# Optimization experiments

Hardware: AMD Instinct MI355X
Metric: run time of the kernel (lower is better)

The kernel has to match this reference:

```python
import jax, jax.numpy as jnp
import numpy as np

N_NODES, N_EDGES, F_IN = 8192, 32768, 16
N_SUB, N_GRAPH = 512, 32
EDGE_DIM, HID = 5, 128
DIMS = [(16, 32), (32, 64), (64, 64)]  # (M_in, M_out) per NNConv layer


def _segment_mean(x, seg, n):
    s = jax.ops.segment_sum(x, seg, num_segments=n)
    c = jax.ops.segment_sum(jnp.ones((x.shape[0], 1), x.dtype), seg, num_segments=n)
    return s / jnp.maximum(c, 1.0)


def _nnconv(x, src, dst, eattr, W1, b1, W2, b2, root, bias):
    # edge MLP -> per-edge weight matrix theta: [E, M_in, M_out]
    h = jax.nn.relu(eattr @ W1 + b1)
    theta = (h @ W2 + b2).reshape(-1, x.shape[1], root.shape[1])
    msg = jnp.einsum('ei,eio->eo', x[src], theta)          # gather + per-edge matvec
    agg = jax.ops.segment_sum(msg, dst, num_segments=x.shape[0])  # scatter-add (aggr='add')
    return agg + x @ root + bias


def setup_inputs() -> dict:
    key = jax.random.key(0)
    ks = jax.random.split(key, 32)
    inp = {}
    inp['x'] = jax.random.normal(ks[0], (N_NODES, F_IN), jnp.float32)
    inp['edge_index'] = jax.random.randint(ks[1], (2, N_EDGES), 0, N_NODES)
    inp['edge_attr'] = jax.random.uniform(ks[2], (N_EDGES, EDGE_DIM), jnp.float32)
    inp['node_to_subgraph'] = jnp.sort(jax.random.randint(ks[3], (N_NODES,), 0, N_SUB))
    inp['subgraph_to_graph'] = jnp.sort(jax.random.randint(ks[4], (N_SUB,), 0, N_GRAPH))
    i = 5
    for l, (ci, co) in enumerate(DIMS):
        inp[f'W1_{l}'] = jax.random.normal(ks[i], (EDGE_DIM, HID), jnp.float32) * 0.1
        inp[f'b1_{l}'] = jnp.zeros((HID,), jnp.float32)
        inp[f'W2_{l}'] = jax.random.normal(ks[i + 1], (HID, ci * co), jnp.float32) * 0.05
        inp[f'b2_{l}'] = jnp.zeros((ci * co,), jnp.float32)
        inp[f'root_{l}'] = jax.random.normal(ks[i + 2], (ci, co), jnp.float32) * 0.1
        inp[f'bias_{l}'] = jnp.zeros((co,), jnp.float32)
        i += 3
    inp['fc1_w'] = jax.random.normal(ks[i], (64, 32), jnp.float32) * 0.1
    inp['fc1_b'] = jnp.zeros((32,), jnp.float32)
    inp['fc2_w'] = jax.random.normal(ks[i + 1], (32, 16), jnp.float32) * 0.1
    inp['fc2_b'] = jnp.zeros((16,), jnp.float32)
    inp['fc3_w'] = jax.random.normal(ks[i + 2], (16, 1), jnp.float32) * 0.1
    inp['fc3_b'] = jnp.zeros((1,), jnp.float32)
    return inp


def reference(x, edge_index, edge_attr, node_to_subgraph, subgraph_to_graph,
              W1_0, b1_0, W2_0, b2_0, root_0, bias_0,
              W1_1, b1_1, W2_1, b2_1, root_1, bias_1,
              W1_2, b1_2, W2_2, b2_2, root_2, bias_2,
              fc1_w, fc1_b, fc2_w, fc2_b, fc3_w, fc3_b):
    src, dst = edge_index[0], edge_index[1]
    layers = [(W1_0, b1_0, W2_0, b2_0, root_0, bias_0),
              (W1_1, b1_1, W2_1, b2_1, root_1, bias_1),
              (W1_2, b1_2, W2_2, b2_2, root_2, bias_2)]
    h = x
    for (W1, b1, W2, b2, root, bias) in layers:
        h = jax.nn.elu(_nnconv(h, src, dst, edge_attr, W1, b1, W2, b2, root, bias))
    h = _segment_mean(h, node_to_subgraph, N_SUB)      # global_mean_pool over subgraphs
    h = _segment_mean(h, subgraph_to_graph, N_GRAPH)   # global_mean_pool over graphs
    h = jax.nn.elu(h @ fc1_w + fc1_b)
    h = jax.nn.elu(h @ fc2_w + fc2_b)
    return (h @ fc3_w + fc3_b).reshape(-1)
```

## Files before the change

kernel.cpp:

```cpp
#include <hip/hip_runtime.h>

#define E_EDGES 32768
#define NN 8192
#define HID 128
#define KS 4

typedef _Float16 half8 __attribute__((ext_vector_type(8)));
typedef _Float16 half4 __attribute__((ext_vector_type(4)));
typedef float f32x4 __attribute__((ext_vector_type(4)));

__global__ void zero_init_k(int* __restrict__ hist, float* __restrict__ pools, int npool) {
  int t = blockIdx.x * 256 + threadIdx.x;
  if (t < NN) hist[t] = 0;
  if (t < npool) pools[t] = 0.f;
}

__global__ void hist_k(const int* __restrict__ dst, int* __restrict__ hist) {
  int e = blockIdx.x * 256 + threadIdx.x;
  if (e < E_EDGES) atomicAdd(&hist[dst[e]], 1);
}

__global__ void scan_k(const int* __restrict__ hist, int* __restrict__ roff, int* __restrict__ cursor) {
  __shared__ int ps[1024];
  int t = threadIdx.x;
  int loc[8]; int s = 0;
  int base = t * 8;
#pragma unroll
  for (int j = 0; j < 8; ++j) { loc[j] = s; s += hist[base + j]; }
  ps[t] = s;
  __syncthreads();
  for (int off = 1; off < 1024; off <<= 1) {
    int v = 0;
    if (t >= off) v = ps[t - off];
    __syncthreads();
    if (t >= off) ps[t] += v;
    __syncthreads();
  }
  int excl = (t == 0) ? 0 : ps[t - 1];
#pragma unroll
  for (int j = 0; j < 8; ++j) { int v = excl + loc[j]; roff[base + j] = v; cursor[base + j] = v; }
  if (t == 1023) roff[NN] = ps[1023];
}

__global__ void scatter_k(const int* __restrict__ dst, int* __restrict__ cursor, int* __restrict__ eidx) {
  int e = blockIdx.x * 256 + threadIdx.x;
  if (e < E_EDGES) { int p = atomicAdd(&cursor[dst[e]], 1); eidx[p] = e; }
}

template <int CI, int CO>
__global__ void prep_b_k(const float* __restrict__ W2, const float* __restrict__ b2,
                         _Float16* __restrict__ out) {
  constexpr int Kmain = 128 * CI;
  constexpr int SPLITK = 32 * CI;
  constexpr int TAILK = ((SPLITK + CI + 127) / 128) * 128;
  constexpr int Kpad = 3 * SPLITK + TAILK;
  int idx = blockIdx.x * 256 + threadIdx.x;
  if (idx >= Kpad * CO) return;
  int j = idx & 7;
  int n = (idx >> 3) & (CO - 1);
  int kg = idx >> (3 + (CO == 64 ? 6 : 5));
  int k = kg * 8 + j;
  float v = 0.f;
  if (k < Kmain) {
    int h = k / CI, i = k & (CI - 1);
    v = W2[(h * CI + i) * CO + n];
  } else if (k < Kmain + CI) {
    int tt = k - Kmain;
    v = b2[tt * CO + n];
  }
  out[idx] = (_Float16)v;
}

template <int CI, int CO>
__launch_bounds__(256, 2)
__global__ void msg_mfma_k(const float* __restrict__ xcur, const int* __restrict__ src,
                           const float* __restrict__ eattr, const float* __restrict__ W1,
                           const float* __restrict__ b1, const _Float16* __restrict__ Bsw,
                           float* __restrict__ msgbuf) {
  constexpr int ME = 256;
  constexpr int L2CI = (CI == 64) ? 6 : ((CI == 32) ? 5 : 4);
  constexpr int Kmain = 128 * CI;
  constexpr int SPLITK = 32 * CI;
  constexpr int TAILK = ((SPLITK + CI + 127) / 128) * 128;
  constexpr int XSTR = CI + 8;
  constexpr int FC = CO / 16;
  constexpr int C4 = CI / 4;
  constexpr int L2C4 = L2CI - 2;

  __shared__ _Float16 he_s[32 * ME];
  __shared__ _Float16 xs_s[ME * XSTR];
  __shared__ float ea_s[ME * 5];
  __shared__ float W1s[5 * 32];
  __shared__ float b1s[32];
  __shared__ int src_s[ME];

  int t = threadIdx.x;
  int e0 = blockIdx.x * ME;
  int y = blockIdx.y;
  int hbeg = y * 32;

  for (int j = t; j < ME * 5; j += 256) ea_s[j] = eattr[e0 * 5 + j];
  if (t < 5 * 32) W1s[t] = W1[(t >> 5) * HID + hbeg + (t & 31)];
  if (t < 32) b1s[t] = b1[hbeg + t];
  src_s[t] = src[e0 + t];
  __syncthreads();

  for (int j = t; j < 32 * ME; j += 256) {
    int hl = j / ME, e = j & (ME - 1);
    float v = b1s[hl];
#pragma unroll
    for (int d = 0; d < 5; ++d) v += ea_s[e * 5 + d] * W1s[d * 32 + hl];
    he_s[hl * ME + e] = (_Float16)fmaxf(v, 0.f);
  }
  for (int j = t; j < ME * C4; j += 256) {
    int e = j >> L2C4, i4 = j & (C4 - 1);
    float4 v = ((const float4*)xcur)[src_s[e] * C4 + i4];
    half4 hq = {(_Float16)v.x, (_Float16)v.y, (_Float16)v.z, (_Float16)v.w};
    *(half4*)&xs_s[e * XSTR + i4 * 4] = hq;
  }
  __syncthreads();

  int lane = t & 63;
  int w = t >> 6;
  int quad = lane >> 4, l15 = lane & 15;

  int cbeg = y * (SPLITK / 32);
  int cend = cbeg + ((y < 3) ? (SPLITK / 32) : (TAILK / 32));
  int nrounds = (cend - cbeg) >> 2;

  const half8* bsw8 = (const half8*)Bsw;
  int ib = quad * CO + l15;

  f32x4 acc[4][FC];
#pragma unroll
  for (int fr = 0; fr < 4; ++fr)
#pragma unroll
    for (int fc = 0; fc < FC; ++fc)
#pragma unroll
      for (int r = 0; r < 4; ++r) acc[fr][fc][r] = 0.f;

  half8 breg[4][FC];
#pragma unroll
  for (int j = 0; j < 4; ++j)
#pragma unroll
    for (int fc = 0; fc < FC; ++fc)
      breg[j][fc] = bsw8[(cbeg + j) * 4 * CO + ib + fc * 16];

  for (int r = 0; r < nrounds; ++r) {
#pragma unroll
    for (int j = 0; j < 4; ++j) {
      int c = cbeg + r * 4 + j;
      int kq = c * 32 + quad * 8;
      int i = kq & (CI - 1);
      int hr = (kq >> L2CI) - hbeg;
      half8 a[4];
#pragma unroll
      for (int fr = 0; fr < 4; ++fr) {
        int e = w * 64 + fr * 16 + l15;
        half8 xv = *(const half8*)&xs_s[e * XSTR + i];
        _Float16 hv = (_Float16)1.f;
        if (kq < Kmain) hv = he_s[hr * ME + e];
        a[fr] = xv * hv;
      }
#pragma unroll
      for (int fc = 0; fc < FC; ++fc) {
#pragma unroll
        for (int fr = 0; fr < 4; ++fr)
          acc[fr][fc] = __builtin_amdgcn_mfma_f32_16x16x32_f16(a[fr], breg[j][fc], acc[fr][fc], 0, 0, 0);
      }
      int cn = c + 4;
      if (cn >= cend) cn = cend - 1;
#pragma unroll
      for (int fc = 0; fc < FC; ++fc)
        breg[j][fc] = bsw8[cn * 4 * CO + ib + fc * 16];
    }
  }

  float* mb = msgbuf + ((size_t)y * E_EDGES + e0) * CO;
#pragma unroll
  for (int fr = 0; fr < 4; ++fr)
#pragma unroll
    for (int fc = 0; fc < FC; ++fc)
#pragma unroll
      for (int r = 0; r < 4; ++r) {
        int el = w * 64 + fr * 16 + quad * 4 + r;
        int o = fc * 16 + l15;
        mb[el * CO + o] = acc[fr][fc][r];
      }
}

template <int CI, int CO>
__global__ void gather_elu_k(const float* __restrict__ xcur, const float* __restrict__ root,
                             const float* __restrict__ bias, const float* __restrict__ msgbuf,
                             const int* __restrict__ roff, const int* __restrict__ eidx,
                             float* __restrict__ xnext) {
  constexpr int NB = 256 / CO;
  __shared__ float xs[NB * CI];
  int t = threadIdx.x;
  int n0 = blockIdx.x * NB;
  for (int j = t; j < NB * CI; j += 256) xs[j] = xcur[n0 * CI + j];
  __syncthreads();
  int nl = t / CO, o = t & (CO - 1);
  int n = n0 + nl;
  float a = bias[o];
#pragma unroll
  for (int i = 0; i < CI; ++i) a += xs[nl * CI + i] * root[i * CO + o];
  int j1 = roff[n + 1];
  for (int j = roff[n]; j < j1; ++j) {
    int e = eidx[j];
    float m = 0.f;
#pragma unroll
    for (int s = 0; s < KS; ++s) m += msgbuf[((size_t)s * E_EDGES + e) * CO + o];
    a += m;
  }
  xnext[n * CO + o] = a > 0.f ? a : expm1f(a);
}

__global__ void pool_sub_k(const float* __restrict__ x3, const int* __restrict__ n2s,
                           float* __restrict__ ssum, float* __restrict__ scnt) {
  int idx = blockIdx.x * 256 + threadIdx.x;
  int n = idx >> 6, o = idx & 63;
  int s = n2s[n];
  atomicAdd(&ssum[(s << 6) + o], x3[idx]);
  if (o == 0) atomicAdd(&scnt[s], 1.f);
}

__global__ void pool_graph_k(const float* __restrict__ ssum, const float* __restrict__ scnt,
                             const int* __restrict__ s2g, float* __restrict__ gsum,
                             float* __restrict__ gcnt) {
  int idx = blockIdx.x * 256 + threadIdx.x;
  int s = idx >> 6, o = idx & 63;
  int g = s2g[s];
  float v = ssum[idx] / fmaxf(scnt[s], 1.f);
  atomicAdd(&gsum[(g << 6) + o], v);
  if (o == 0) atomicAdd(&gcnt[g], 1.f);
}

__global__ void head_k(const float* __restrict__ gsum, const float* __restrict__ gcnt,
                       const float* __restrict__ w1, const float* __restrict__ b1,
                       const float* __restrict__ w2, const float* __restrict__ b2,
                       const float* __restrict__ w3, const float* __restrict__ b3,
                       float* __restrict__ out) {
  int g = blockIdx.x;
  int t = threadIdx.x;
  __shared__ float m[64], s1[32], s2[16];
  float c = fmaxf(gcnt[g], 1.f);
  m[t] = gsum[g * 64 + t] / c;
  __syncthreads();
  if (t < 32) {
    float a = b1[t];
    for (int i = 0; i < 64; ++i) a += m[i] * w1[i * 32 + t];
    s1[t] = a > 0.f ? a : expm1f(a);
  }
  __syncthreads();
  if (t < 16) {
    float a = b2[t];
    for (int i = 0; i < 32; ++i) a += s1[i] * w2[i * 16 + t];
    s2[t] = a > 0.f ? a : expm1f(a);
  }
  __syncthreads();
  if (t == 0) {
    float a = b3[0];
    for (int i = 0; i < 16; ++i) a += s2[i] * w3[i];
    out[g] = a;
  }
}

extern "C" void kernel_launch(void* const* d_in, const int* in_sizes, int n_in,
                              void* d_out, int out_size, void* d_ws, size_t ws_size,
                              hipStream_t stream) {
  (void)in_sizes; (void)n_in; (void)out_size; (void)ws_size;
  const float* x0 = (const float*)d_in[0];
  const int* ei = (const int*)d_in[1];
  const float* ea = (const float*)d_in[2];
  const int* n2s = (const int*)d_in[3];
  const int* s2g = (const int*)d_in[4];
  const float* W1_[3] = {(const float*)d_in[5], (const float*)d_in[11], (const float*)d_in[17]};
  const float* b1_[3] = {(const float*)d_in[6], (const float*)d_in[12], (const float*)d_in[18]};
  const float* W2_[3] = {(const float*)d_in[7], (const float*)d_in[13], (const float*)d_in[19]};
  const float* b2_[3] = {(const float*)d_in[8], (const float*)d_in[14], (const float*)d_in[20]};
  const float* rt_[3] = {(const float*)d_in[9], (const float*)d_in[15], (const float*)d_in[21]};
  const float* bs_[3] = {(const float*)d_in[10], (const float*)d_in[16], (const float*)d_in[22]};
  const float* fc1w = (const float*)d_in[23]; const float* fc1b = (const float*)d_in[24];
  const float* fc2w = (const float*)d_in[25]; const float* fc2b = (const float*)d_in[26];
  const float* fc3w = (const float*)d_in[27]; const float* fc3b = (const float*)d_in[28];
  float* out = (float*)d_out;

  const int* srcp = ei;
  const int* dstp = ei + E_EDGES;

  char* wsb = (char*)d_ws;
  size_t off = 0;
  auto alloc = [&](size_t bytes) {
    void* p = wsb + off;
    off += (bytes + 255) & ~(size_t)255;
    return p;
  };
  _Float16* Bsw0 = (_Float16*)alloc((size_t)2176 * 32 * 2);
  _Float16* Bsw1 = (_Float16*)alloc((size_t)4224 * 64 * 2);
  _Float16* Bsw2 = (_Float16*)alloc((size_t)8320 * 64 * 2);
  float* msgbuf = (float*)alloc((size_t)KS * E_EDGES * 64 * 4);
  float* x1 = (float*)alloc((size_t)NN * 32 * 4);
  float* x2 = (float*)alloc((size_t)NN * 64 * 4);
  float* x3 = (float*)alloc((size_t)NN * 64 * 4);
  int* hist = (int*)alloc((size_t)NN * 4);
  int* roff = (int*)alloc((size_t)(NN + 1) * 4);
  int* cursor = (int*)alloc((size_t)NN * 4);
  int* eidx = (int*)alloc((size_t)E_EDGES * 4);
  const int npool = 512 * 64 + 512 + 32 * 64 + 32;
  float* pools = (float*)alloc((size_t)npool * 4);
  float* ssum = pools;
  float* scnt = pools + 512 * 64;
  float* gsum = scnt + 512;
  float* gcnt = gsum + 32 * 64;

  zero_init_k<<<(npool + 255) / 256, 256, 0, stream>>>(hist, pools, npool);
  hist_k<<<E_EDGES / 256, 256, 0, stream>>>(dstp, hist);
  scan_k<<<1, 1024, 0, stream>>>(hist, roff, cursor);
  scatter_k<<<E_EDGES / 256, 256, 0, stream>>>(dstp, cursor, eidx);
  prep_b_k<16, 32><<<(2176 * 32 + 255) / 256, 256, 0, stream>>>(W2_[0], b2_[0], Bsw0);
  prep_b_k<32, 64><<<(4224 * 64 + 255) / 256, 256, 0, stream>>>(W2_[1], b2_[1], Bsw1);
  prep_b_k<64, 64><<<(8320 * 64 + 255) / 256, 256, 0, stream>>>(W2_[2], b2_[2], Bsw2);

  dim3 mg(E_EDGES / 256, KS);
  msg_mfma_k<16, 32><<<mg, 256, 0, stream>>>(x0, srcp, ea, W1_[0], b1_[0], Bsw0, msgbuf);
  gather_elu_k<16, 32><<<NN / 8, 256, 0, stream>>>(x0, rt_[0], bs_[0], msgbuf, roff, eidx, x1);
  msg_mfma_k<32, 64><<<mg, 256, 0, stream>>>(x1, srcp, ea, W1_[1], b1_[1], Bsw1, msgbuf);
  gather_elu_k<32, 64><<<NN / 4, 256, 0, stream>>>(x1, rt_[1], bs_[1], msgbuf, roff, eidx, x2);
  msg_mfma_k<64, 64><<<mg, 256, 0, stream>>>(x2, srcp, ea, W1_[2], b1_[2], Bsw2, msgbuf);
  gather_elu_k<64, 64><<<NN / 4, 256, 0, stream>>>(x2, rt_[2], bs_[2], msgbuf, roff, eidx, x3);

  pool_sub_k<<<NN * 64 / 256, 256, 0, stream>>>(x3, n2s, ssum, scnt);
  pool_graph_k<<<512 * 64 / 256, 256, 0, stream>>>(ssum, scnt, s2g, gsum, gcnt);
  head_k<<<32, 64, 0, stream>>>(gsum, gcnt, fc1w, fc1b, fc2w, fc2b, fc3w, fc3b, out);
}
```

Baseline: 269.6 us.

## Fuse CSR build and weight prep kernels, hoist x fragments into registers

Merges zero-init, histogram and scan into one single-block kernel that builds the histogram in shared memory, and merges the three per-layer weight-prep launches into one kernel. This cuts launch count and launch overhead. In the message kernel, each lane's x fragments are loaded from LDS into registers once instead of being reloaded for every K chunk. The cost is a histogram done by one workgroup and extra register pressure.

```diff
diff --git a/kernel.cpp b/kernel.cpp
--- a/kernel.cpp
+++ b/kernel.cpp
@@ -9,24 +9,20 @@
 typedef _Float16 half4 __attribute__((ext_vector_type(4)));
 typedef float f32x4 __attribute__((ext_vector_type(4)));
 
-__global__ void zero_init_k(int* __restrict__ hist, float* __restrict__ pools, int npool) {
-  int t = blockIdx.x * 256 + threadIdx.x;
-  if (t < NN) hist[t] = 0;
-  if (t < npool) pools[t] = 0.f;
-}
-
-__global__ void hist_k(const int* __restrict__ dst, int* __restrict__ hist) {
-  int e = blockIdx.x * 256 + threadIdx.x;
-  if (e < E_EDGES) atomicAdd(&hist[dst[e]], 1);
-}
-
-__global__ void scan_k(const int* __restrict__ hist, int* __restrict__ roff, int* __restrict__ cursor) {
+__global__ void csr_scan_k(const int* __restrict__ dst, float* __restrict__ pools,
+                           int npool, int* __restrict__ roff, int* __restrict__ cursor) {
+  __shared__ int h[NN];
   __shared__ int ps[1024];
   int t = threadIdx.x;
+  for (int j = t; j < NN; j += 1024) h[j] = 0;
+  for (int j = t; j < npool; j += 1024) pools[j] = 0.f;
+  __syncthreads();
+  for (int j = t; j < E_EDGES; j += 1024) atomicAdd(&h[dst[j]], 1);
+  __syncthreads();
   int loc[8]; int s = 0;
   int base = t * 8;
 #pragma unroll
-  for (int j = 0; j < 8; ++j) { loc[j] = s; s += hist[base + j]; }
+  for (int j = 0; j < 8; ++j) { loc[j] = s; s += h[base + j]; }
   ps[t] = s;
   __syncthreads();
   for (int off = 1; off < 1024; off <<= 1) {
@@ -47,28 +43,34 @@
   if (e < E_EDGES) { int p = atomicAdd(&cursor[dst[e]], 1); eidx[p] = e; }
 }
 
-template <int CI, int CO>
-__global__ void prep_b_k(const float* __restrict__ W2, const float* __restrict__ b2,
-                         _Float16* __restrict__ out) {
-  constexpr int Kmain = 128 * CI;
-  constexpr int SPLITK = 32 * CI;
-  constexpr int TAILK = ((SPLITK + CI + 127) / 128) * 128;
-  constexpr int Kpad = 3 * SPLITK + TAILK;
-  int idx = blockIdx.x * 256 + threadIdx.x;
-  if (idx >= Kpad * CO) return;
+__device__ __forceinline__ void prep_one(int idx, int l2ci, int l2co,
+                                         const float* __restrict__ W2,
+                                         const float* __restrict__ b2,
+                                         _Float16* __restrict__ out) {
+  int CI = 1 << l2ci, CO = 1 << l2co;
+  int Kmain = CI << 7;
   int j = idx & 7;
   int n = (idx >> 3) & (CO - 1);
-  int kg = idx >> (3 + (CO == 64 ? 6 : 5));
+  int kg = idx >> (3 + l2co);
   int k = kg * 8 + j;
   float v = 0.f;
   if (k < Kmain) {
-    int h = k / CI, i = k & (CI - 1);
-    v = W2[(h * CI + i) * CO + n];
+    int hh = k >> l2ci, i = k & (CI - 1);
+    v = W2[((hh << l2ci) + i) * CO + n];
   } else if (k < Kmain + CI) {
-    int tt = k - Kmain;
-    v = b2[tt * CO + n];
+    v = b2[(k - Kmain) * CO + n];
   }
   out[idx] = (_Float16)v;
+}
+
+__global__ void prep_all_k(const float* __restrict__ W2a, const float* __restrict__ b2a, _Float16* __restrict__ oa,
+                           const float* __restrict__ W2b, const float* __restrict__ b2b, _Float16* __restrict__ ob,
+                           const float* __restrict__ W2c, const float* __restrict__ b2c, _Float16* __restrict__ oc) {
+  const int s0 = 2176 * 32, s1 = 4224 * 64, s2 = 8320 * 64;
+  int idx = blockIdx.x * 256 + threadIdx.x;
+  if (idx < s0) prep_one(idx, 4, 5, W2a, b2a, oa);
+  else if (idx < s0 + s1) prep_one(idx - s0, 5, 6, W2b, b2b, ob);
+  else if (idx < s0 + s1 + s2) prep_one(idx - s0 - s1, 6, 6, W2c, b2c, oc);
 }
 
 template <int CI, int CO>
@@ -86,6 +88,7 @@
   constexpr int FC = CO / 16;
   constexpr int C4 = CI / 4;
   constexpr int L2C4 = L2CI - 2;
+  constexpr int NV = (CI == 64) ? 2 : 1;
 
   __shared__ _Float16 he_s[32 * ME];
   __shared__ _Float16 xs_s[ME * XSTR];
@@ -124,6 +127,14 @@
   int w = t >> 6;
   int quad = lane >> 4, l15 = lane & 15;
 
+  half8 xreg[4][NV];
+#pragma unroll
+  for (int fr = 0; fr < 4; ++fr)
+#pragma unroll
+    for (int v = 0; v < NV; ++v)
+      xreg[fr][v] = *(const half8*)&xs_s[(w * 64 + fr * 16 + l15) * XSTR +
+                                         ((quad * 8 + v * 32) & (CI - 1))];
+
   int cbeg = y * (SPLITK / 32);
   int cend = cbeg + ((y < 3) ? (SPLITK / 32) : (TAILK / 32));
   int nrounds = (cend - cbeg) >> 2;
@@ -151,16 +162,16 @@
     for (int j = 0; j < 4; ++j) {
       int c = cbeg + r * 4 + j;
       int kq = c * 32 + quad * 8;
-      int i = kq & (CI - 1);
       int hr = (kq >> L2CI) - hbeg;
+      constexpr int PAR = (CI == 64) ? 1 : 0;
+      int vi = PAR ? (j & 1) : 0;
       half8 a[4];
 #pragma unroll
       for (int fr = 0; fr < 4; ++fr) {
         int e = w * 64 + fr * 16 + l15;
-        half8 xv = *(const half8*)&xs_s[e * XSTR + i];
         _Float16 hv = (_Float16)1.f;
         if (kq < Kmain) hv = he_s[hr * ME + e];
-        a[fr] = xv * hv;
+        a[fr] = xreg[fr][vi] * hv;
       }
 #pragma unroll
       for (int fc = 0; fc < FC; ++fc) {
@@ -303,7 +314,6 @@
   float* x1 = (float*)alloc((size_t)NN * 32 * 4);
   float* x2 = (float*)alloc((size_t)NN * 64 * 4);
   float* x3 = (float*)alloc((size_t)NN * 64 * 4);
-  int* hist = (int*)alloc((size_t)NN * 4);
   int* roff = (int*)alloc((size_t)(NN + 1) * 4);
   int* cursor = (int*)alloc((size_t)NN * 4);
   int* eidx = (int*)alloc((size_t)E_EDGES * 4);
@@ -314,13 +324,12 @@
   float* gsum = scnt + 512;
   float* gcnt = gsum + 32 * 64;
 
-  zero_init_k<<<(npool + 255) / 256, 256, 0, stream>>>(hist, pools, npool);
-  hist_k<<<E_EDGES / 256, 256, 0, stream>>>(dstp, hist);
-  scan_k<<<1, 1024, 0, stream>>>(hist, roff, cursor);
+  csr_scan_k<<<1, 1024, 0, stream>>>(dstp, pools, npool, roff, cursor);
   scatter_k<<<E_EDGES / 256, 256, 0, stream>>>(dstp, cursor, eidx);
-  prep_b_k<16, 32><<<(2176 * 32 + 255) / 256, 256, 0, stream>>>(W2_[0], b2_[0], Bsw0);
-  prep_b_k<32, 64><<<(4224 * 64 + 255) / 256, 256, 0, stream>>>(W2_[1], b2_[1], Bsw1);
-  prep_b_k<64, 64><<<(8320 * 64 + 255) / 256, 256, 0, stream>>>(W2_[2], b2_[2], Bsw2);
+  const int preptot = 2176 * 32 + 4224 * 64 + 8320 * 64;
+  prep_all_k<<<(preptot + 255) / 256, 256, 0, stream>>>(W2_[0], b2_[0], Bsw0,
+                                                        W2_[1], b2_[1], Bsw1,
+                                                        W2_[2], b2_[2], Bsw2);
 
   dim3 mg(E_EDGES / 256, KS);
   msg_mfma_k<16, 32><<<mg, 256, 0, stream>>>(x0, srcp, ea, W1_[0], b1_[0], Bsw0, msgbuf);
```

Result: no change. 271.1 us (+0.6%).
